# Optimization experiments

Hardware: AMD Instinct MI355X
Metric: run time of the kernel (lower is better)

The kernel has to match this reference:

```python
import jax, jax.numpy as jnp
import numpy as np

B, R, T = 32, 256, 4096  # shots, receivers, time samples; P = T prob grid
EPS = 1e-8


def _trapz(y, t):
    # trapezoidal integral along last axis
    dt = t[1:] - t[:-1]
    return jnp.sum(0.5 * (y[..., 1:] + y[..., :-1]) * dt, axis=-1)


def _cum_trap(y, t):
    # cumulative trapezoid along last axis, prepend 0 -> same length as y
    dt = t[1:] - t[:-1]
    incr = 0.5 * (y[..., 1:] + y[..., :-1]) * dt
    c = jnp.cumsum(incr, axis=-1)
    return jnp.concatenate([jnp.zeros_like(c[..., :1]), c], axis=-1)


def _renorm(x, t):
    # square + trapz-normalize each trace to a probability density over t
    pdf = x * x + EPS
    return pdf / _trapz(pdf, t)[..., None]


def setup_inputs() -> dict:
    key = jax.random.key(0)
    k1, k2 = jax.random.split(key)
    traces = 0.5 * jax.random.normal(k1, (B, R, T), dtype=jnp.float32)
    t = jnp.arange(T, dtype=jnp.float32) * 1e-3
    p = jnp.linspace(0.0, 1.0, T, dtype=jnp.float32)  # probability grid
    # q_raw = true_quantile(obs_data, t, p): invert the observed CDF per trace
    obs = 0.5 * jax.random.normal(k2, (B, R, T), dtype=jnp.float32)
    obs_pdf = _renorm(obs, t)
    obs_cdf = _cum_trap(obs_pdf, t)  # strictly increasing (pdf > 0)
    q_raw = jax.vmap(lambda c: jnp.interp(p, c, t))(obs_cdf.reshape(-1, T))
    q_raw = q_raw.reshape(B, R, T).astype(jnp.float32)
    return {"traces": traces, "t": t, "p": p, "q_raw": q_raw}


def reference(traces, t, p, q_raw):
    pdf = _renorm(traces, t)          # [B,R,T]
    cdf = _cum_trap(pdf, t)           # [B,R,T], in [0,1]
    # quantile lookup: interpolate each trace's quantile table at its cdf values
    cdf_f = cdf.reshape(-1, T)
    q_f = q_raw.reshape(-1, T)
    transport = jax.vmap(jnp.interp, in_axes=(0, None, 0))(cdf_f, p, q_f)
    transport = transport.reshape(pdf.shape)
    diff = t - transport
    loss = jnp.sum(_trapz(diff * diff * pdf, t))
    return loss
```

## Files before the change

kernel.cpp:

```cpp
#include <hip/hip_runtime.h>

#define TT 4096
#define BLK 256
#define PER 16
#define EPSV 1e-8f

__global__ __launch_bounds__(BLK) void w2_loss_kernel(
    const float* __restrict__ traces,
    const float* __restrict__ q_raw,
    float* __restrict__ part) {
  __shared__ float lds_q[TT];
  __shared__ float wave_sums[4];
  __shared__ float wave_red[4];

  const int tid = threadIdx.x;
  const long trace = blockIdx.x;
  const float* __restrict__ tr = traces + trace * TT;
  const float* __restrict__ qr = q_raw + trace * TT;

  const int base = tid * PER;

  float4 trv[4];
  {
    const float4* tr4 = (const float4*)(tr + base);
#pragma unroll
    for (int j = 0; j < 4; ++j) trv[j] = tr4[j];
  }
  float nb = (base + PER < TT) ? tr[base + PER] : 0.0f;

  {
    const float4* q4 = (const float4*)qr;
    float4* lq4 = (float4*)lds_q;
#pragma unroll
    for (int j = 0; j < 4; ++j) lq4[tid + BLK * j] = q4[tid + BLK * j];
  }

  float s[PER + 1];
#pragma unroll
  for (int j = 0; j < 4; ++j) {
    s[4 * j + 0] = trv[j].x * trv[j].x + EPSV;
    s[4 * j + 1] = trv[j].y * trv[j].y + EPSV;
    s[4 * j + 2] = trv[j].z * trv[j].z + EPSV;
    s[4 * j + 3] = trv[j].w * trv[j].w + EPSV;
  }
  s[PER] = (base + PER < TT) ? (nb * nb + EPSV) : 0.0f;

  float lc[PER + 1];
  lc[0] = 0.0f;
#pragma unroll
  for (int m = 0; m < PER; ++m) {
    float t0 = (float)(base + m) * 1e-3f;
    float t1 = (float)(base + m + 1) * 1e-3f;
    float incr = (base + m < TT - 1) ? 0.5f * (s[m] + s[m + 1]) * (t1 - t0)
                                     : 0.0f;
    lc[m + 1] = lc[m] + incr;
  }
  const float tot = lc[PER];

  float v = tot;
#pragma unroll
  for (int off = 1; off < 64; off <<= 1) {
    float n = __shfl_up(v, off, 64);
    if ((tid & 63) >= off) v += n;
  }
  if ((tid & 63) == 63) wave_sums[tid >> 6] = v;
  __syncthreads();

  const int wv = tid >> 6;
  float wave_off = 0.0f;
  if (wv > 0) wave_off += wave_sums[0];
  if (wv > 1) wave_off += wave_sums[1];
  if (wv > 2) wave_off += wave_sums[2];
  const float excl = (v - tot) + wave_off;
  const float norm = wave_sums[0] + wave_sums[1] + wave_sums[2] + wave_sums[3];
  const float inv_norm = 1.0f / norm;

  float local = 0.0f;
#pragma unroll
  for (int m = 0; m < PER; ++m) {
    float x = (excl + lc[m]) * inv_norm;
    float u = x * (float)(TT - 1);
    int i0 = (int)floorf(u);
    i0 = (i0 < 0) ? 0 : ((i0 > TT - 2) ? TT - 2 : i0);
    float f = u - (float)i0;
    f = fminf(fmaxf(f, 0.0f), 1.0f);
    float q0 = lds_q[i0];
    float q1 = lds_q[i0 + 1];
    float transport = q0 + f * (q1 - q0);
    float tm = (float)(base + m) * 1e-3f;
    float d = tm - transport;
    float tlo = (float)((base + m == 0) ? 0 : (base + m - 1)) * 1e-3f;
    float thi = (float)((base + m == TT - 1) ? (TT - 1) : (base + m + 1)) * 1e-3f;
    float w = 0.5f * (thi - tlo);
    local += d * d * s[m] * w;
  }
  local *= inv_norm;

#pragma unroll
  for (int off = 32; off > 0; off >>= 1) local += __shfl_down(local, off, 64);
  if ((tid & 63) == 0) wave_red[tid >> 6] = local;
  __syncthreads();
  if (tid == 0) {
    part[blockIdx.x] = wave_red[0] + wave_red[1] + wave_red[2] + wave_red[3];
  }
}

__global__ __launch_bounds__(BLK) void reduce_kernel(
    const float* __restrict__ part, float* __restrict__ out, int n) {
  __shared__ float wave_red[4];
  const int tid = threadIdx.x;
  float local = 0.0f;
  for (int i = tid; i < n; i += BLK) local += part[i];
#pragma unroll
  for (int off = 32; off > 0; off >>= 1) local += __shfl_down(local, off, 64);
  if ((tid & 63) == 0) wave_red[tid >> 6] = local;
  __syncthreads();
  if (tid == 0) out[0] = wave_red[0] + wave_red[1] + wave_red[2] + wave_red[3];
}

extern "C" void kernel_launch(void* const* d_in, const int* in_sizes, int n_in,
                              void* d_out, int out_size, void* d_ws, size_t ws_size,
                              hipStream_t stream) {
  const float* traces = (const float*)d_in[0];
  const float* q_raw  = (const float*)d_in[3];
  float* out = (float*)d_out;
  float* part = (float*)d_ws;

  const int n_traces = in_sizes[0] / TT;
  w2_loss_kernel<<<n_traces, BLK, 0, stream>>>(traces, q_raw, part);
  reduce_kernel<<<1, BLK, 0, stream>>>(part, out, n_traces);
}
```

Baseline: 284.1 us.

## Process one trace per wavefront with chunked scans and direct global quantile gathers

Each wavefront now handles a whole trace in 16 coalesced float4 chunks. It computes the cumulative trapezoid with per-chunk wave scans and a running carry, so LDS staging of q_raw and block-level barriers are no longer needed. The trace is read twice, once for the normalisation scan and once for the loss pass. Quantile values are gathered straight from global memory instead of LDS. This removes syncthreads and LDS traffic but adds a second read of the traces, 16 serial wave scans per trace, and random global gathers that rely on cache hits.

```diff
diff --git a/kernel.cpp b/kernel.cpp
--- a/kernel.cpp
+++ b/kernel.cpp
@@ -2,107 +2,116 @@
 
 #define TT 4096
 #define BLK 256
-#define PER 16
+#define WPB 4
+#define CHUNKS 16
 #define EPSV 1e-8f
 
-__global__ __launch_bounds__(BLK) void w2_loss_kernel(
+__device__ __forceinline__ float tf(int i) { return (float)i * 1e-3f; }
+
+__global__ __launch_bounds__(BLK, 8) void w2_loss_kernel(
     const float* __restrict__ traces,
     const float* __restrict__ q_raw,
     float* __restrict__ part) {
-  __shared__ float lds_q[TT];
-  __shared__ float wave_sums[4];
-  __shared__ float wave_red[4];
-
-  const int tid = threadIdx.x;
-  const long trace = blockIdx.x;
+  const int lane = threadIdx.x & 63;
+  const int wid  = threadIdx.x >> 6;
+  const long trace = (long)blockIdx.x * WPB + wid;
   const float* __restrict__ tr = traces + trace * TT;
   const float* __restrict__ qr = q_raw + trace * TT;
+  const float4* __restrict__ tr4 = (const float4*)tr;
 
-  const int base = tid * PER;
-
-  float4 trv[4];
-  {
-    const float4* tr4 = (const float4*)(tr + base);
+  float base[CHUNKS];
+  float running = 0.0f;
+  float4 cur = tr4[lane];
 #pragma unroll
-    for (int j = 0; j < 4; ++j) trv[j] = tr4[j];
+  for (int k = 0; k < CHUNKS; ++k) {
+    float4 nxt = (k + 1 < CHUNKS) ? tr4[(k + 1) * 64 + lane]
+                                  : make_float4(0.f, 0.f, 0.f, 0.f);
+    float s0 = cur.x * cur.x + EPSV;
+    float s1 = cur.y * cur.y + EPSV;
+    float s2 = cur.z * cur.z + EPSV;
+    float s3 = cur.w * cur.w + EPSV;
+    float snx = nxt.x * nxt.x + EPSV;
+    float nb = __shfl_down(s0, 1, 64);
+    float bc = __shfl(snx, 0, 64);
+    float s4 = (lane == 63) ? bc : nb;
+    int e = k * 256 + lane * 4;
+    float i0 = 0.5f * (s0 + s1) * (tf(e + 1) - tf(e));
+    float i1 = 0.5f * (s1 + s2) * (tf(e + 2) - tf(e + 1));
+    float i2 = 0.5f * (s2 + s3) * (tf(e + 3) - tf(e + 2));
+    float i3 = (e + 3 < TT - 1) ? 0.5f * (s3 + s4) * (tf(e + 4) - tf(e + 3)) : 0.0f;
+    float lt = i0 + i1 + i2 + i3;
+    float v = lt;
+#pragma unroll
+    for (int off = 1; off < 64; off <<= 1) {
+      float n = __shfl_up(v, off, 64);
+      if (lane >= off) v += n;
+    }
+    base[k] = running + (v - lt);
+    running += __shfl(v, 63, 64);
+    cur = nxt;
   }
-  float nb = (base + PER < TT) ? tr[base + PER] : 0.0f;
-
-  {
-    const float4* q4 = (const float4*)qr;
-    float4* lq4 = (float4*)lds_q;
-#pragma unroll
-    for (int j = 0; j < 4; ++j) lq4[tid + BLK * j] = q4[tid + BLK * j];
-  }
-
-  float s[PER + 1];
-#pragma unroll
-  for (int j = 0; j < 4; ++j) {
-    s[4 * j + 0] = trv[j].x * trv[j].x + EPSV;
-    s[4 * j + 1] = trv[j].y * trv[j].y + EPSV;
-    s[4 * j + 2] = trv[j].z * trv[j].z + EPSV;
-    s[4 * j + 3] = trv[j].w * trv[j].w + EPSV;
-  }
-  s[PER] = (base + PER < TT) ? (nb * nb + EPSV) : 0.0f;
-
-  float lc[PER + 1];
-  lc[0] = 0.0f;
-#pragma unroll
-  for (int m = 0; m < PER; ++m) {
-    float t0 = (float)(base + m) * 1e-3f;
-    float t1 = (float)(base + m + 1) * 1e-3f;
-    float incr = (base + m < TT - 1) ? 0.5f * (s[m] + s[m + 1]) * (t1 - t0)
-                                     : 0.0f;
-    lc[m + 1] = lc[m] + incr;
-  }
-  const float tot = lc[PER];
-
-  float v = tot;
-#pragma unroll
-  for (int off = 1; off < 64; off <<= 1) {
-    float n = __shfl_up(v, off, 64);
-    if ((tid & 63) >= off) v += n;
-  }
-  if ((tid & 63) == 63) wave_sums[tid >> 6] = v;
-  __syncthreads();
-
-  const int wv = tid >> 6;
-  float wave_off = 0.0f;
-  if (wv > 0) wave_off += wave_sums[0];
-  if (wv > 1) wave_off += wave_sums[1];
-  if (wv > 2) wave_off += wave_sums[2];
-  const float excl = (v - tot) + wave_off;
-  const float norm = wave_sums[0] + wave_sums[1] + wave_sums[2] + wave_sums[3];
-  const float inv_norm = 1.0f / norm;
+  const float inv_norm = 1.0f / running;
 
   float local = 0.0f;
+  cur = tr4[lane];
 #pragma unroll
-  for (int m = 0; m < PER; ++m) {
-    float x = (excl + lc[m]) * inv_norm;
-    float u = x * (float)(TT - 1);
-    int i0 = (int)floorf(u);
-    i0 = (i0 < 0) ? 0 : ((i0 > TT - 2) ? TT - 2 : i0);
-    float f = u - (float)i0;
-    f = fminf(fmaxf(f, 0.0f), 1.0f);
-    float q0 = lds_q[i0];
-    float q1 = lds_q[i0 + 1];
-    float transport = q0 + f * (q1 - q0);
-    float tm = (float)(base + m) * 1e-3f;
-    float d = tm - transport;
-    float tlo = (float)((base + m == 0) ? 0 : (base + m - 1)) * 1e-3f;
-    float thi = (float)((base + m == TT - 1) ? (TT - 1) : (base + m + 1)) * 1e-3f;
-    float w = 0.5f * (thi - tlo);
-    local += d * d * s[m] * w;
+  for (int k = 0; k < CHUNKS; ++k) {
+    float4 nxt = (k + 1 < CHUNKS) ? tr4[(k + 1) * 64 + lane]
+                                  : make_float4(0.f, 0.f, 0.f, 0.f);
+    float s0 = cur.x * cur.x + EPSV;
+    float s1 = cur.y * cur.y + EPSV;
+    float s2 = cur.z * cur.z + EPSV;
+    float s3 = cur.w * cur.w + EPSV;
+    float snx = nxt.x * nxt.x + EPSV;
+    float nb = __shfl_down(s0, 1, 64);
+    float bc = __shfl(snx, 0, 64);
+    float s4 = (lane == 63) ? bc : nb;
+    int e = k * 256 + lane * 4;
+    float i0 = 0.5f * (s0 + s1) * (tf(e + 1) - tf(e));
+    float i1 = 0.5f * (s1 + s2) * (tf(e + 2) - tf(e + 1));
+    float i2 = 0.5f * (s2 + s3) * (tf(e + 3) - tf(e + 2));
+    float c[4];
+    c[0] = base[k];
+    c[1] = c[0] + i0;
+    c[2] = c[1] + i1;
+    c[3] = c[2] + i2;
+    float sv[4] = {s0, s1, s2, s3};
+
+    int ix[4];
+    float fr[4];
+#pragma unroll
+    for (int j = 0; j < 4; ++j) {
+      float x = c[j] * inv_norm;
+      float u = x * (float)(TT - 1);
+      int i0i = (int)floorf(u);
+      i0i = (i0i < 0) ? 0 : ((i0i > TT - 2) ? TT - 2 : i0i);
+      float f = u - (float)i0i;
+      ix[j] = i0i;
+      fr[j] = fminf(fmaxf(f, 0.0f), 1.0f);
+    }
+    float q0v[4], q1v[4];
+#pragma unroll
+    for (int j = 0; j < 4; ++j) {
+      q0v[j] = qr[ix[j]];
+      q1v[j] = qr[ix[j] + 1];
+    }
+#pragma unroll
+    for (int j = 0; j < 4; ++j) {
+      float transport = q0v[j] + fr[j] * (q1v[j] - q0v[j]);
+      int ei = e + j;
+      float d = tf(ei) - transport;
+      float tlo = tf((ei == 0) ? 0 : ei - 1);
+      float thi = tf((ei == TT - 1) ? (TT - 1) : ei + 1);
+      float w = 0.5f * (thi - tlo);
+      local += d * d * sv[j] * w;
+    }
+    cur = nxt;
   }
   local *= inv_norm;
 
 #pragma unroll
   for (int off = 32; off > 0; off >>= 1) local += __shfl_down(local, off, 64);
-  if ((tid & 63) == 0) wave_red[tid >> 6] = local;
-  __syncthreads();
-  if (tid == 0) {
-    part[blockIdx.x] = wave_red[0] + wave_red[1] + wave_red[2] + wave_red[3];
-  }
+  if (lane == 0) part[trace] = local;
 }
 
 __global__ __launch_bounds__(BLK) void reduce_kernel(
@@ -127,6 +136,6 @@
   float* part = (float*)d_ws;
 
   const int n_traces = in_sizes[0] / TT;
-  w2_loss_kernel<<<n_traces, BLK, 0, stream>>>(traces, q_raw, part);
+  w2_loss_kernel<<<n_traces / WPB, BLK, 0, stream>>>(traces, q_raw, part);
   reduce_kernel<<<1, BLK, 0, stream>>>(part, out, n_traces);
 }
```

Measured after the change: 471.2 us. 1.66x slower.
